# Kernel tuning notes

Hardware: AMD Instinct MI355X
Metric: run time of the kernel (lower is better)

## Reference

```python
import math
import jax, jax.numpy as jnp
import numpy as np

B, N, D = 8, 2048, 256
NUM_ROLES = 3
ROLE_HUB, ROLE_MONITOR = 1, 2  # assumed ROLE_TO_ID mapping
NEG = -10000.0


def _lin_init(k, fan_in, shape):
    b = 1.0 / math.sqrt(fan_in)
    return jax.random.uniform(k, shape, jnp.float32, -b, b)


def setup_inputs() -> dict:
    key = jax.random.key(0)
    ks = jax.random.split(key, 20)
    inp = {
        'x': jax.random.normal(ks[0], (B, N, D), jnp.float32),
        'node_roles': jax.random.randint(ks[1], (B, N), 0, NUM_ROLES),
        'node_mask': jax.random.bernoulli(ks[2], 0.9, (B, N)),
        'ln_gamma': jnp.ones((D,), jnp.float32),
        'ln_beta': jnp.zeros((D,), jnp.float32),
        'role_emb': jax.random.normal(ks[3], (NUM_ROLES, D), jnp.float32),
    }
    names = ['q', 'k', 's', 'p', 'o']
    for i, nm in enumerate(names):
        inp['W' + nm] = _lin_init(ks[4 + 2 * i], D, (D, D))
        inp['b' + nm] = _lin_init(ks[5 + 2 * i], D, (D,))
    inp['Wg'] = _lin_init(ks[14], 2 * D, (2 * D, D))
    inp['bg'] = _lin_init(ks[15], 2 * D, (D,))
    return inp


def _layernorm(x, g, b):
    mu = jnp.mean(x, -1, keepdims=True)
    var = jnp.mean(jnp.square(x - mu), -1, keepdims=True)
    return (x - mu) * jax.lax.rsqrt(var + 1e-5) * g + b


def reference(x, node_roles, node_mask, ln_gamma, ln_beta, role_emb,
              Wq, bq, Wk, bk, Ws, bs, Wp, bp, Wo, bo, Wg, bg):
    normed = _layernorm(x, ln_gamma, ln_beta)
    role_bias = role_emb[node_roles]                      # [B,N,D]
    h = normed + role_bias
    query = h @ Wq + bq
    key_t = h @ Wk + bk
    sender = h @ Ws + bs
    payload = normed @ Wp + bp

    read_logits = jnp.einsum('bid,bjd->bij', query, key_t) / math.sqrt(D)
    fs = role_bias + sender
    forward_logits = jnp.einsum('bid,bjd->bij', fs, fs)
    logits = read_logits + 0.5 * forward_logits           # variant='selective'

    source_mask = node_mask                               # variant != 'memory_hubs'
    pair_mask = node_mask[:, :, None] & source_mask[:, None, :]
    eye = jnp.eye(N, dtype=bool)[None]
    pair_mask = pair_mask | (eye & node_mask[:, :, None] & node_mask[:, None, :])

    logits = jnp.where(pair_mask, logits, NEG)
    weights = jax.nn.softmax(logits, axis=-1)
    weights = jnp.where(pair_mask, weights, 0.0)

    message = jnp.einsum('bij,bjd->bid', weights, payload)
    gate = jax.nn.sigmoid(jnp.concatenate([x, message], axis=-1) @ Wg + bg)
    update = (gate * message) @ Wo + bo
    out = x + update                                      # dropout p=0

    entropy = -(weights * jnp.log(weights + 1e-8)).sum(-1).mean()
    # masked-mean replicates torch's weights[..., col_mask].mean() without dynamic shapes
    mon_cols = (node_roles == ROLE_MONITOR).any(0)        # [N]
    hub_cols = (node_roles == ROLE_HUB).any(0)
    def col_mean(cols):
        cnt = cols.sum() * B * N
        tot = (weights * cols[None, None, :].astype(weights.dtype)).sum()
        return jnp.where(cnt > 0, tot / jnp.maximum(cnt, 1), 0.0)
    return (out, entropy, col_mean(mon_cols), col_mean(hub_cols))
```

## Files before the change

kernel.cpp:

```cpp
#include <hip/hip_runtime.h>
#include <math.h>

#define BB 8
#define NN 2048
#define DD 256
#define MTOK 16384

typedef __bf16 bf16x8 __attribute__((ext_vector_type(8)));
typedef __bf16 bf16x4 __attribute__((ext_vector_type(4)));
typedef float f32x4 __attribute__((ext_vector_type(4)));

#define MFMA16(a, b, c) __builtin_amdgcn_mfma_f32_16x16x32_bf16(a, b, c, 0, 0, 0)

#define BARX()                              \
  do {                                      \
    asm volatile("" ::: "memory");          \
    __builtin_amdgcn_s_barrier();           \
    asm volatile("" ::: "memory");          \
  } while (0)
#define WAITVM(N)                                              \
  do {                                                         \
    asm volatile("s_waitcnt vmcnt(" #N ")" ::: "memory");      \
    __builtin_amdgcn_sched_barrier(0);                         \
  } while (0)

#define OFF_X16    0ull
#define OFF_N16    2097152ull
#define OFF_H16    4194304ull
#define OFF_GROW   8388608ull
#define OFF_GCOL   12582912ull
#define OFF_PTE    16777216ull
#define OFF_WT     19005440ull
#define OFF_STAT   19234816ull
#define OFF_ENT    23625728ull
#define OFF_MONR   23642112ull
#define OFF_HUBR   23658496ull
#define OFF_MONF   23674880ull
#define OFF_HUBF   23676928ull
#define OFF_MASK   23678976ull
#define OFF_PART   23683072ull
#define OFF_MSGN0  OFF_N16
#define OFF_MSGN1  OFF_H16
#define OFF_MSG16  OFF_PTE
#define OFF_GM16   OFF_GROW

__device__ __forceinline__ void gl_lds16(const void* g, void* l) {
  __builtin_amdgcn_global_load_lds(
      (const __attribute__((address_space(1))) unsigned int*)g,
      (__attribute__((address_space(3))) unsigned int*)l, 16, 0, 0);
}

__global__ __launch_bounds__(256) void setup_kernel(
    const float* __restrict__ x, const int* __restrict__ roles,
    const void* __restrict__ mraw,
    const float* __restrict__ gamma, const float* __restrict__ beta,
    const float* __restrict__ role_emb,
    const float* __restrict__ Wq, const float* __restrict__ Wk,
    const float* __restrict__ Ws, const float* __restrict__ Wp,
    const float* __restrict__ Wg, const float* __restrict__ Wo,
    __bf16* __restrict__ X16, __bf16* __restrict__ N16,
    __bf16* __restrict__ H16, __bf16* __restrict__ WT,
    unsigned char* __restrict__ mask8,
    float* __restrict__ monf, float* __restrict__ hubf,
    __bf16* __restrict__ PTE) {
  __shared__ float T[64][65];
  int bid = blockIdx.x;
  int tid = threadIdx.x;
  if (bid < 4096) {
    int t = bid * 4 + (tid >> 6);
    int lane = tid & 63;
    size_t off = (size_t)t * DD + lane * 4;
    float4 xv = *(const float4*)(x + off);
    float s = xv.x + xv.y + xv.z + xv.w;
    float ss = xv.x * xv.x + xv.y * xv.y + xv.z * xv.z + xv.w * xv.w;
#pragma unroll
    for (int m = 1; m < 64; m <<= 1) {
      s += __shfl_xor(s, m, 64);
      ss += __shfl_xor(ss, m, 64);
    }
    float mu = s * (1.0f / 256.0f);
    float var = ss * (1.0f / 256.0f) - mu * mu;
    float inv = rsqrtf(var + 1e-5f);
    float4 g = *(const float4*)(gamma + lane * 4);
    float4 be = *(const float4*)(beta + lane * 4);
    float nv[4];
    nv[0] = (xv.x - mu) * inv * g.x + be.x;
    nv[1] = (xv.y - mu) * inv * g.y + be.y;
    nv[2] = (xv.z - mu) * inv * g.z + be.z;
    nv[3] = (xv.w - mu) * inv * g.w + be.w;
    int role = roles[t];
    float4 rb = *(const float4*)(role_emb + (size_t)role * DD + lane * 4);
    float rbv[4] = {rb.x, rb.y, rb.z, rb.w};
    bf16x4 xo, no, ho;
    float xf[4] = {xv.x, xv.y, xv.z, xv.w};
#pragma unroll
    for (int q = 0; q < 4; ++q) {
      xo[q] = (__bf16)xf[q];
      no[q] = (__bf16)nv[q];
      ho[q] = (__bf16)(nv[q] + rbv[q]);
    }
    *(bf16x4*)&X16[off] = xo;
    *(bf16x4*)&N16[off] = no;
    *(bf16x4*)&H16[off] = ho;
  } else if (bid < 4288) {
    int wblk = bid - 4096;
    int z = wblk >> 5, rem = wblk & 31;
    int bx = rem & 3, by = rem >> 2;
    const float* src;
    int K;
    size_t doff;
    switch (z) {
      case 0: src = Wq; K = 256; doff = 0; break;
      case 1: src = Wk; K = 256; doff = 65536; break;
      case 2: src = Ws; K = 256; doff = 131072; break;
      case 3: src = Wp; K = 256; doff = 196608; break;
      case 4: src = Wg; K = 512; doff = 262144; break;
      default: src = Wo; K = 256; doff = 393216; break;
    }
    int k0 = by * 64;
    if (k0 >= K) return;
    int n0 = bx * 64;
#pragma unroll
    for (int p = 0; p < 16; ++p) {
      int idx = p * 256 + tid;
      int r = idx >> 6, c = idx & 63;
      T[r][c] = src[(size_t)(k0 + r) * 256 + n0 + c];
    }
    __syncthreads();
#pragma unroll
    for (int p = 0; p < 16; ++p) {
      int idx = p * 256 + tid;
      int n = idx >> 6, k = idx & 63;
      WT[doff + (size_t)(n0 + n) * K + k0 + k] = (__bf16)T[k][n];
    }
  } else if (bid < 4352) {
    int* csh = (int*)&T[0][0];
    if (tid == 0) { csh[0] = 0; csh[1] = 0; }
    __syncthreads();
    const unsigned char* raw = (const unsigned char*)mraw;
    int c0 = 0, c1 = 0;
    for (int i = tid; i < 4096; i += 256) {
      int nz = (raw[i] != 0) ? 1 : 0;
      if ((i & 3) == 0) c0 += nz; else c1 += nz;
    }
    atomicAdd(&csh[0], c0);
    atomicAdd(&csh[1], c1);
    __syncthreads();
    int k = (csh[0] == 0) ? 2 : ((csh[1] == 0) ? 0 : 1);
    int t = (bid - 4288) * 256 + tid;
    if (t < MTOK) {
      int v;
      if (k == 1)      v = (raw[t] != 0);
      else if (k == 0) v = (((const int*)mraw)[t] != 0);
      else             v = (((const float*)mraw)[t] != 0.0f);
      mask8[t] = (unsigned char)v;
    }
    if (t < NN) {
      int mon = 0, hub = 0;
#pragma unroll
      for (int b = 0; b < BB; ++b) {
        int r = roles[b * NN + t];
        mon |= (r == 2) ? 1 : 0;
        hub |= (r == 1) ? 1 : 0;
      }
      monf[t] = (float)mon;
      hubf[t] = (float)hub;
    }
  } else {
    int idx = (bid - 4352) * 256 + tid;
    int b = idx >> 11, col = idx & 2047;
    int mon = 0, hub = 0;
#pragma unroll
    for (int bb = 0; bb < BB; ++bb) {
      int r = roles[bb * NN + col];
      mon |= (r == 2) ? 1 : 0;
      hub |= (r == 1) ? 1 : 0;
    }
    size_t rbase = ((size_t)(b * 272 + 256)) * 2048 + col;
    PTE[rbase] = (__bf16)(float)mon;
    PTE[rbase + 2048] = (__bf16)(float)hub;
    PTE[rbase + 2 * 2048] = (__bf16)1.0f;
#pragma unroll
    for (int r = 3; r < 16; ++r) PTE[rbase + (size_t)r * 2048] = (__bf16)0.0f;
  }
}

__global__ __launch_bounds__(256, 4) void proj4_kernel(
    const __bf16* __restrict__ H16, const __bf16* __restrict__ N16,
    const __bf16* __restrict__ WT,
    const float* __restrict__ bq, const float* __restrict__ bk,
    const float* __restrict__ bs, const float* __restrict__ bp,
    const int* __restrict__ roles, const float* __restrict__ remb,
    __bf16* __restrict__ Grow, __bf16* __restrict__ Gcol,
    __bf16* __restrict__ PTE) {
  __shared__ __align__(16) unsigned char As[128 * 128];
  __shared__ __align__(16) unsigned char Bs[128 * 128];
  int z = blockIdx.z;
  const __bf16* A = (z == 3) ? N16 : H16;
  const __bf16* W = WT + (size_t)z * 65536;
  const float* bias = (z == 0) ? bq : (z == 1) ? bk : (z == 2) ? bs : bp;

  int tid = threadIdx.x;
  int w = tid >> 6, lane = tid & 63, ln15 = lane & 15, lq = lane >> 4;
  int wr = w >> 1, wc = w & 1;
  int row0 = blockIdx.y * 128, col0 = blockIdx.x * 128;
  f32x4 acc[4][4];
#pragma unroll
  for (int i = 0; i < 4; ++i)
#pragma unroll
    for (int j = 0; j < 4; ++j) acc[i][j] = (f32x4){0.f, 0.f, 0.f, 0.f};

  int lr = lane >> 3;
  int sb = ((lane & 7) * 16) ^ ((lr & 7) << 4);

  for (int kt = 0; kt < 4; ++kt) {
    __syncthreads();
#pragma unroll
    for (int i2 = 0; i2 < 4; ++i2) {
      int idx = w * 4 + i2;
      int grow = row0 + idx * 8 + lr;
      gl_lds16((const unsigned char*)A + (size_t)grow * 512 + kt * 128 + sb,
               As + idx * 1024);
    }
#pragma unroll
    for (int i2 = 0; i2 < 4; ++i2) {
      int idx = w * 4 + i2;
      int gcol = col0 + idx * 8 + lr;
      gl_lds16((const unsigned char*)W + (size_t)gcol * 512 + kt * 128 + sb,
               Bs + idx * 1024);
    }
    __syncthreads();
#pragma unroll
    for (int ks = 0; ks < 2; ++ks) {
      bf16x8 af[4], bfr[4];
#pragma unroll
      for (int i = 0; i < 4; ++i) {
        int rl = wr * 64 + i * 16 + ln15;
        int byteoff = (lq * 16 + ks * 64) ^ ((rl & 7) << 4);
        af[i] = *(const bf16x8*)(As + rl * 128 + byteoff);
      }
#pragma unroll
      for (int j = 0; j < 4; ++j) {
        int cl = wc * 64 + j * 16 + ln15;
        int byteoff = (lq * 16 + ks * 64) ^ ((cl & 7) << 4);
        bfr[j] = *(const bf16x8*)(Bs + cl * 128 + byteoff);
      }
#pragma unroll
      for (int i = 0; i < 4; ++i)
#pragma unroll
        for (int j = 0; j < 4; ++j) acc[i][j] = MFMA16(af[i], bfr[j], acc[i][j]);
    }
  }
  float bj[4];
#pragma unroll
  for (int j = 0; j < 4; ++j) bj[j] = bias[col0 + wc * 64 + j * 16 + ln15];
#pragma unroll
  for (int i = 0; i < 4; ++i) {
#pragma unroll
    for (int j = 0; j < 4; ++j) {
      int gcol = col0 + wc * 64 + j * 16 + ln15;
      int growb = row0 + wr * 64 + i * 16 + lq * 4;
      float o[4];
#pragma unroll
      for (int ri = 0; ri < 4; ++ri) o[ri] = acc[i][j][ri] + bj[j];
      if (z == 0) {
#pragma unroll
        for (int ri = 0; ri < 4; ++ri)
          Grow[(size_t)(growb + ri) * 512 + gcol] = (__bf16)(o[ri] * 0.0625f);
      } else if (z == 1) {
#pragma unroll
        for (int ri = 0; ri < 4; ++ri)
          Gcol[(size_t)(growb + ri) * 512 + gcol] = (__bf16)o[ri];
      } else if (z == 2) {
#pragma unroll
        for (int ri = 0; ri < 4; ++ri) {
          float oo = o[ri] + remb[(size_t)roles[growb + ri] * 256 + gcol];
          Grow[(size_t)(growb + ri) * 512 + 256 + gcol] =
              (__bf16)(oo * 0.70710678118f);
        }
      } else {
        bf16x4 v;
#pragma unroll
        for (int ri = 0; ri < 4; ++ri) v[ri] = (__bf16)o[ri];
        int b = growb >> 11, tok = growb & 2047;
        *(bf16x4*)&PTE[((size_t)(b * 272 + gcol)) * 2048 + tok] = v;
      }
    }
  }
}

__global__ __launch_bounds__(256, 2) void attn_kernel(
    const __bf16* __restrict__ Grow, const __bf16* __restrict__ Gcol,
    const __bf16* __restrict__ PTE, const unsigned char* __restrict__ mask8,
    __bf16* __restrict__ msgn0, __bf16* __restrict__ msgn1,
    float* __restrict__ statP) {
  __shared__ __align__(16) unsigned char GcLo[16384];
  __shared__ __align__(16) unsigned char GcHi[16384];
  __shared__ __align__(16) unsigned char PtS[2][17408];

  int tid = threadIdx.x;
  int w = tid >> 6, lane = tid & 63, ln15 = lane & 15, lq = lane >> 4;
  int id = blockIdx.x;
  int b = id & 7;
  int half = (id >> 3) & 1;
  int r0 = (id >> 4) * 64;
  size_t base = (size_t)b * NN;
  __bf16* msgn = half ? msgn1 : msgn0;
  float* statB = statP + (size_t)half * MTOK * 6;

  const unsigned char* gbaseK =
      (const unsigned char*)Gcol + (base + half * 1024) * 1024;
  const unsigned char* gbaseF =
      (const unsigned char*)Grow + (base + half * 1024) * 1024;
  const unsigned char* pbase =
      (const unsigned char*)PTE + (size_t)b * 272 * 4096 + half * 2048;

  bf16x8 Af[16];
  {
    const __bf16* gr = Grow + (base + r0 + w * 16 + ln15) * 512 + lq * 8;
#pragma unroll
    for (int kk = 0; kk < 16; ++kk) Af[kk] = *(const bf16x8*)(gr + kk * 32);
  }

  float m = -1e30f, T = 0.f;
  f32x4 macc[17];
#pragma unroll
  for (int nt = 0; nt < 17; ++nt) macc[nt] = (f32x4){0.f, 0.f, 0.f, 0.f};

  int pswz = (lq ^ ((ln15 >> 1) & 3)) << 4;
  int n0 = ((ln15 >> 2) * 8) + (ln15 & 3);
  int n1 = n0 + 4;
  int s0 = (((n0 & 3) | (((n0 >> 3) & 1) << 2))) << 4;
  int s1 = (((n1 & 3) | (((n1 >> 3) & 1) << 2))) << 4;
  int srcsw = ((lane & 3) ^ ((lane >> 3) & 3)) << 4;
  int glrow = lane >> 5;
  int glb = (lane & 31) * 16;

  auto STG = [&](const unsigned char* gb, int ch, unsigned char* dst, int koff) {
#pragma unroll
    for (int i = 0; i < 4; ++i) {
      int rp = w * 8 + 2 * i;
      int r = rp + glrow;
      int sbr = glb ^ ((((r & 3) | (((r >> 3) & 1) << 2))) << 4);
      gl_lds16(gb + (size_t)(ch * 32 + r) * 1024 + koff + sbr, dst + rp * 512);
    }
  };
  auto STPT = [&](int ch, int buf) {
#pragma unroll
    for (int i = 0; i < 4; ++i) {
      int idx = w * 4 + i;
      int drow = idx * 16 + (lane >> 2);
      gl_lds16(pbase + (size_t)drow * 4096 + ch * 64 + srcsw,
               &PtS[buf][idx * 1024]);
    }
    {
      int drow = 256 + (lane >> 2);
      gl_lds16(pbase + (size_t)drow * 4096 + ch * 64 + srcsw,
               &PtS[buf][16 * 1024]);
    }
  };

  STPT(0, 0);
  STG(gbaseK, 0, GcLo, 0);
  STG(gbaseF, 0, GcHi, 512);

  for (int ch = 0; ch < 32; ++ch) {
    int cur = ch & 1;
    WAITVM(4);
    BARX();
    STPT(ch + 1, cur ^ 1);

    f32x4 sa0 = (f32x4){0.f, 0.f, 0.f, 0.f};
    f32x4 sa1 = (f32x4){0.f, 0.f, 0.f, 0.f};
    __builtin_amdgcn_s_setprio(1);
#pragma unroll
    for (int kk = 0; kk < 8; ++kk) {
      bf16x8 bv0 = *(const bf16x8*)&GcLo[n0 * 512 + ((lq * 16 + kk * 64) ^ s0)];
      sa0 = MFMA16(bv0, Af[kk], sa0);
      bf16x8 bv1 = *(const bf16x8*)&GcLo[n1 * 512 + ((lq * 16 + kk * 64) ^ s1)];
      sa1 = MFMA16(bv1, Af[kk], sa1);
    }
    __builtin_amdgcn_s_setprio(0);

    WAITVM(5);
    BARX();
    STG(gbaseK, ch + 1, GcLo, 0);

    __builtin_amdgcn_s_setprio(1);
#pragma unroll
    for (int kk = 8; kk < 16; ++kk) {
      bf16x8 bv0 = *(const bf16x8*)&GcHi[n0 * 512 + ((lq * 16 + (kk - 8) * 64) ^ s0)];
      sa0 = MFMA16(bv0, Af[kk], sa0);
      bf16x8 bv1 = *(const bf16x8*)&GcHi[n1 * 512 + ((lq * 16 + (kk - 8) * 64) ^ s1)];
      sa1 = MFMA16(bv1, Af[kk], sa1);
    }
    __builtin_amdgcn_s_setprio(0);

    float sv[8] = {sa0[0], sa0[1], sa0[2], sa0[3], sa1[0], sa1[1], sa1[2], sa1[3]};
    unsigned long long mk = *(const unsigned long long*)(
        mask8 + base + half * 1024 + (size_t)ch * 32 + lq * 8);

    float mt = -1e30f;
#pragma unroll
    for (int i = 0; i < 8; ++i) {
      float li = ((mk >> (8 * i)) & 0xffull) ? sv[i] : -1e30f;
      mt = fmaxf(mt, li);
    }
    mt = fmaxf(mt, __shfl_xor(mt, 16));
    mt = fmaxf(mt, __shfl_xor(mt, 32));
    float mnew = fmaxf(m, mt);
    if (__any(mnew > m + 8.0f)) {
      float ci = __expf(m - mnew);
      float cir[4];
#pragma unroll
      for (int r = 0; r < 4; ++r)
        cir[r] = __shfl(ci, (lane & 48) + ((lane >> 2) & 12) + r);
#pragma unroll
      for (int nt = 0; nt < 17; ++nt) {
        macc[nt][0] *= cir[0]; macc[nt][1] *= cir[1];
        macc[nt][2] *= cir[2]; macc[nt][3] *= cir[3];
      }
      T *= ci;
      m = mnew;
    }
    float e[8], tl = 0.f;
#pragma unroll
    for (int i = 0; i < 8; ++i) {
      float ei = ((mk >> (8 * i)) & 0xffull) ? __expf(sv[i] - m) : 0.f;
      e[i] = ei;
      tl += ei * sv[i];
    }
    tl += __shfl_xor(tl, 16);
    tl += __shfl_xor(tl, 32);
    T += tl;
    bf16x8 ef;
#pragma unroll
    for (int i = 0; i < 8; ++i) ef[i] = (__bf16)e[i];

    __builtin_amdgcn_s_setprio(1);
#pragma unroll
    for (int nt = 0; nt < 17; ++nt) {
      int drow = nt * 16 + ln15;
      bf16x8 pv = *(const bf16x8*)&PtS[cur][drow * 64 + pswz];
      macc[nt] = MFMA16(ef, pv, macc[nt]);
    }
    __builtin_amdgcn_s_setprio(0);

    BARX();
    STG(gbaseF, ch + 1, GcHi, 512);
  }
  WAITVM(0);

#pragma unroll
  for (int r = 0; r < 4; ++r) {
    int grow = r0 + w * 16 + lq * 4 + r;
    size_t row = base + grow;
    float Z = __shfl(macc[16][r], (lane & 48) + 2);
    float invZ = (Z > 0.f) ? (1.0f / Z) : 0.f;
#pragma unroll
    for (int nt = 0; nt < 16; ++nt)
      msgn[row * 256 + nt * 16 + ln15] = (__bf16)(macc[nt][r] * invZ);
    float Tm = __shfl(macc[16][r], (lane & 48) + 0);
    float Th = __shfl(macc[16][r], (lane & 48) + 1);
    float Tr = __shfl(T, (lane & 48) + ((lane >> 2) & 12) + r);
    float mr = __shfl(m, (lane & 48) + ((lane >> 2) & 12) + r);
    if (ln15 == 0) {
      float* stt = statB + row * 6;
      stt[0] = mr; stt[1] = Tr; stt[2] = Z; stt[3] = Tm; stt[4] = Th;
    }
  }
}

__global__ __launch_bounds__(256) void merge_kernel(
    const __bf16* __restrict__ msgn0, const __bf16* __restrict__ msgn1,
    const float* __restrict__ statP, const unsigned char* __restrict__ mask8,
    __bf16* __restrict__ MSG16, float* __restrict__ entr,
    float* __restrict__ monr, float* __restrict__ hubr) {
  int row = blockIdx.x * 4 + (threadIdx.x >> 6);
  int lane = threadIdx.x & 63;
  const float* s0 = statP + (size_t)row * 6;
  const float* s1 = statP + (size_t)(MTOK + row) * 6;
  float m0 = s0[0], T0 = s0[1], Z0 = s0[2], Tm0 = s0[3], Th0 = s0[4];
  float m1 = s1[0], T1 = s1[1], Z1 = s1[2], Tm1 = s1[3], Th1 = s1[4];
  int valid = mask8[row] != 0;
  float mm = fmaxf(m0, m1);
  float c0 = __expf(m0 - mm), c1 = __expf(m1 - mm);
  float w0 = c0 * Z0, w1 = c1 * Z1;
  float Z = w0 + w1;
  int ok = valid && (Z > 0.f);
  float invZ = ok ? (1.0f / Z) : 0.0f;
  float rw0 = w0 * invZ, rw1 = w1 * invZ;
  bf16x4 p0 = *(const bf16x4*)(msgn0 + (size_t)row * 256 + lane * 4);
  bf16x4 p1 = *(const bf16x4*)(msgn1 + (size_t)row * 256 + lane * 4);
  bf16x4 o;
#pragma unroll
  for (int q = 0; q < 4; ++q)
    o[q] = (__bf16)(rw0 * (float)p0[q] + rw1 * (float)p1[q]);
  *(bf16x4*)&MSG16[(size_t)row * 256 + lane * 4] = o;
  if (lane == 0) {
    float T = c0 * T0 + c1 * T1;
    float Tm = c0 * Tm0 + c1 * Tm1;
    float Th = c0 * Th0 + c1 * Th1;
    entr[row] = ok ? (__logf(Z) + mm - T * invZ) : 0.0f;
    monr[row] = ok ? (Tm * invZ) : 0.0f;
    hubr[row] = ok ? (Th * invZ) : 0.0f;
  }
}

template <int K, int MODE>
__global__ __launch_bounds__(256) void gemmb_kernel(
    const __bf16* __restrict__ A0, const __bf16* __restrict__ A1,
    const __bf16* __restrict__ WT, const float* __restrict__ bias,
    const float* __restrict__ xf, const __bf16* __restrict__ msg16,
    void* __restrict__ dst0) {
  __shared__ __align__(16) unsigned char As[128 * 128];
  __shared__ __align__(16) unsigned char Bs[64 * 128];
  int tid = threadIdx.x;
  int w = tid >> 6, lane = tid & 63, ln15 = lane & 15, lq = lane >> 4;
  int wr = w >> 1, wc = w & 1;
  int row0 = blockIdx.y * 128, col0 = blockIdx.x * 64;
  f32x4 acc[4][2];
#pragma unroll
  for (int i = 0; i < 4; ++i)
#pragma unroll
    for (int j = 0; j < 2; ++j) acc[i][j] = (f32x4){0.f, 0.f, 0.f, 0.f};

  int lr = lane >> 3;
  int sb = ((lane & 7) * 16) ^ ((lr & 7) << 4);

  for (int kt = 0; kt < K / 64; ++kt) {
    const __bf16* Ab = A0;
    int ktl = kt;
    if (K == 512 && kt >= 4) { Ab = A1; ktl = kt - 4; }
    __syncthreads();
#pragma unroll
    for (int i2 = 0; i2 < 4; ++i2) {
      int idx = w * 4 + i2;
      int grow = row0 + idx * 8 + lr;
      gl_lds16((const unsigned char*)Ab + (size_t)grow * 512 + ktl * 128 + sb,
               As + idx * 1024);
    }
#pragma unroll
    for (int i2 = 0; i2 < 2; ++i2) {
      int idx = w * 2 + i2;
      int gcol = col0 + idx * 8 + lr;
      gl_lds16((const unsigned char*)WT + (size_t)gcol * (K * 2) + kt * 128 + sb,
               Bs + idx * 1024);
    }
    __syncthreads();
#pragma unroll
    for (int ks = 0; ks < 2; ++ks) {
      bf16x8 af[4], bfr[2];
#pragma unroll
      for (int i = 0; i < 4; ++i) {
        int rl = wr * 64 + i * 16 + ln15;
        int byteoff = (lq * 16 + ks * 64) ^ ((rl & 7) << 4);
        af[i] = *(const bf16x8*)(As + rl * 128 + byteoff);
      }
#pragma unroll
      for (int j = 0; j < 2; ++j) {
        int cl = wc * 32 + j * 16 + ln15;
        int byteoff = (lq * 16 + ks * 64) ^ ((cl & 7) << 4);
        bfr[j] = *(const bf16x8*)(Bs + cl * 128 + byteoff);
      }
#pragma unroll
      for (int i = 0; i < 4; ++i)
#pragma unroll
        for (int j = 0; j < 2; ++j) acc[i][j] = MFMA16(af[i], bfr[j], acc[i][j]);
    }
  }
  float bj[2];
#pragma unroll
  for (int j = 0; j < 2; ++j) bj[j] = bias[col0 + wc * 32 + j * 16 + ln15];
#pragma unroll
  for (int i = 0; i < 4; ++i) {
#pragma unroll
    for (int ri = 0; ri < 4; ++ri) {
      int grow = row0 + wr * 64 + i * 16 + lq * 4 + ri;
#pragma unroll
      for (int j = 0; j < 2; ++j) {
        int gcol = col0 + wc * 32 + j * 16 + ln15;
        float o = acc[i][j][ri] + bj[j];
        if (MODE == 4) {
          float sg = 1.0f / (1.0f + __expf(-o));
          float mv = (float)msg16[(size_t)grow * 256 + gcol];
          ((__bf16*)dst0)[(size_t)grow * 256 + gcol] = (__bf16)(sg * mv);
        } else {
          ((float*)dst0)[(size_t)grow * 256 + gcol] =
              o + xf[(size_t)grow * 256 + gcol];
        }
      }
    }
  }
}

__device__ __forceinline__ float block_sum(float v, float* sh) {
  __syncthreads();
  sh[threadIdx.x] = v;
  __syncthreads();
  for (int s = 128; s > 0; s >>= 1) {
    if ((int)threadIdx.x < s) sh[threadIdx.x] += sh[threadIdx.x + s];
    __syncthreads();
  }
  return sh[0];
}

__global__ __launch_bounds__(256) void reduce1_kernel(
    const float* __restrict__ entr, const float* __restrict__ monr,
    const float* __restrict__ hubr, float* __restrict__ partial) {
  __shared__ float sh[256];
  int t = blockIdx.x * 256 + threadIdx.x;
  float es = entr[t], ms = monr[t], hs = hubr[t];
  float e = block_sum(es, sh);
  float mo = block_sum(ms, sh);
  float hu = block_sum(hs, sh);
  if (threadIdx.x == 0) {
    partial[blockIdx.x * 4 + 0] = e;
    partial[blockIdx.x * 4 + 1] = mo;
    partial[blockIdx.x * 4 + 2] = hu;
  }
}

__global__ __launch_bounds__(256) void reduce2_kernel(
    const float* __restrict__ partial, const float* __restrict__ monf,
    const float* __restrict__ hubf, float* __restrict__ out3) {
  __shared__ float sh[256];
  float es = 0.f, ms = 0.f, hs = 0.f, cmf = 0.f, chf = 0.f;
  if (threadIdx.x < 64) {
    es = partial[threadIdx.x * 4 + 0];
    ms = partial[threadIdx.x * 4 + 1];
    hs = partial[threadIdx.x * 4 + 2];
  }
  for (int j = threadIdx.x; j < NN; j += 256) { cmf += monf[j]; chf += hubf[j]; }
  float esum = block_sum(es, sh);
  float msum = block_sum(ms, sh);
  float hsum = block_sum(hs, sh);
  float cmsum = block_sum(cmf, sh);
  float chsum = block_sum(chf, sh);
  if (threadIdx.x == 0) {
    out3[0] = esum / 16384.0f;
    out3[1] = (cmsum > 0.f) ? (msum / (cmsum * 16384.0f)) : 0.0f;
    out3[2] = (chsum > 0.f) ? (hsum / (chsum * 16384.0f)) : 0.0f;
  }
}

extern "C" void kernel_launch(void* const* d_in, const int* in_sizes, int n_in,
                              void* d_out, int out_size, void* d_ws, size_t ws_size,
                              hipStream_t stream) {
  const float* x = (const float*)d_in[0];
  const int* roles = (const int*)d_in[1];
  const void* mraw = d_in[2];
  const float* gamma = (const float*)d_in[3];
  const float* beta = (const float*)d_in[4];
  const float* remb = (const float*)d_in[5];
  const float* Wq = (const float*)d_in[6];
  const float* bq = (const float*)d_in[7];
  const float* Wk = (const float*)d_in[8];
  const float* bk = (const float*)d_in[9];
  const float* Ws = (const float*)d_in[10];
  const float* bs = (const float*)d_in[11];
  const float* Wp = (const float*)d_in[12];
  const float* bp = (const float*)d_in[13];
  const float* Wo = (const float*)d_in[14];
  const float* bo = (const float*)d_in[15];
  const float* Wg = (const float*)d_in[16];
  const float* bg = (const float*)d_in[17];

  float* ws = (float*)d_ws;
  __bf16* X16 = (__bf16*)(ws + OFF_X16);
  __bf16* N16 = (__bf16*)(ws + OFF_N16);
  __bf16* H16 = (__bf16*)(ws + OFF_H16);
  __bf16* Grow = (__bf16*)(ws + OFF_GROW);
  __bf16* Gcol = (__bf16*)(ws + OFF_GCOL);
  __bf16* PTE = (__bf16*)(ws + OFF_PTE);
  __bf16* WT = (__bf16*)(ws + OFF_WT);
  float* statP = ws + OFF_STAT;
  __bf16* msgn0 = (__bf16*)(ws + OFF_MSGN0);
  __bf16* msgn1 = (__bf16*)(ws + OFF_MSGN1);
  float* partial = ws + OFF_PART;
  __bf16* MSG16 = (__bf16*)(ws + OFF_MSG16);
  __bf16* GM16 = (__bf16*)(ws + OFF_GM16);
  float* entr = ws + OFF_ENT;
  float* monr = ws + OFF_MONR;
  float* hubr = ws + OFF_HUBR;
  float* monfp = ws + OFF_MONF;
  float* hubfp = ws + OFF_HUBF;
  unsigned char* mask8 = (unsigned char*)(ws + OFF_MASK);
  float* out = (float*)d_out;

  __bf16* WTg = WT + 262144;
  __bf16* WTo = WT + 393216;

  setup_kernel<<<4416, 256, 0, stream>>>(x, roles, mraw, gamma, beta, remb,
                                         Wq, Wk, Ws, Wp, Wg, Wo,
                                         X16, N16, H16, WT, mask8, monfp,
                                         hubfp, PTE);
  proj4_kernel<<<dim3(2, 128, 4), 256, 0, stream>>>(
      H16, N16, WT, bq, bk, bs, bp, roles, remb, Grow, Gcol, PTE);
  attn_kernel<<<512, 256, 0, stream>>>(Grow, Gcol, PTE, mask8, msgn0, msgn1,
                                       statP);
  merge_kernel<<<4096, 256, 0, stream>>>(msgn0, msgn1, statP, mask8, MSG16,
                                         entr, monr, hubr);
  dim3 gg(4, 128);
  gemmb_kernel<512, 4><<<gg, 256, 0, stream>>>(X16, MSG16, WTg, bg, nullptr,
                                               MSG16, GM16);
  gemmb_kernel<256, 5><<<gg, 256, 0, stream>>>(GM16, nullptr, WTo, bo, x,
                                               nullptr, out);
  reduce1_kernel<<<64, 256, 0, stream>>>(entr, monr, hubr, partial);
  reduce2_kernel<<<1, 256, 0, stream>>>(partial, monfp, hubfp, out + 4194304);
}
```

Before: 163.1 us.

## Switch attention kernel to 32x32 MFMA tiles with 128-row blocks and single-barrier staging

Rewrites the attention kernel to use 32x32x16 bf16 MFMA instead of 16x16x32, giving each wave 32 query rows and each block 128 rows, which halves the grid to 256 blocks. Both key and forward-logit tiles and the payload tile are now double-buffered and staged in one call per chunk with a single barrier, instead of split stages. Probability fragments are repacked across lanes with v_permlane32_swap to match the 32x32 B-operand layout. PTE padding grows from 16 to 32 extra rows so the payload fits 9 tiles of 32, and workspace offsets shift accordingly. The intent is fewer MFMA issues and fewer LDS reads per FLOP. The costs are much larger LDS use and register pressure (occupancy 1 block/CU) and only 256 blocks for the device.

```diff
diff --git a/kernel.cpp b/kernel.cpp
--- a/kernel.cpp
+++ b/kernel.cpp
@@ -9,8 +9,10 @@
 typedef __bf16 bf16x8 __attribute__((ext_vector_type(8)));
 typedef __bf16 bf16x4 __attribute__((ext_vector_type(4)));
 typedef float f32x4 __attribute__((ext_vector_type(4)));
+typedef float f32x16 __attribute__((ext_vector_type(16)));
 
 #define MFMA16(a, b, c) __builtin_amdgcn_mfma_f32_16x16x32_bf16(a, b, c, 0, 0, 0)
+#define MFMA32(a, b, c) __builtin_amdgcn_mfma_f32_32x32x16_bf16(a, b, c, 0, 0, 0)
 
 #define BARX()                              \
   do {                                      \
@@ -30,8 +32,8 @@
 #define OFF_GROW   8388608ull
 #define OFF_GCOL   12582912ull
 #define OFF_PTE    16777216ull
-#define OFF_WT     19005440ull
-#define OFF_STAT   19234816ull
+#define OFF_WT     19136512ull
+#define OFF_STAT   19365888ull
 #define OFF_ENT    23625728ull
 #define OFF_MONR   23642112ull
 #define OFF_HUBR   23658496ull
@@ -176,12 +178,12 @@
       mon |= (r == 2) ? 1 : 0;
       hub |= (r == 1) ? 1 : 0;
     }
-    size_t rbase = ((size_t)(b * 272 + 256)) * 2048 + col;
+    size_t rbase = ((size_t)(b * 288 + 256)) * 2048 + col;
     PTE[rbase] = (__bf16)(float)mon;
     PTE[rbase + 2048] = (__bf16)(float)hub;
     PTE[rbase + 2 * 2048] = (__bf16)1.0f;
 #pragma unroll
-    for (int r = 3; r < 16; ++r) PTE[rbase + (size_t)r * 2048] = (__bf16)0.0f;
+    for (int r = 3; r < 32; ++r) PTE[rbase + (size_t)r * 2048] = (__bf16)0.0f;
   }
 }
 
@@ -283,27 +285,29 @@
 #pragma unroll
         for (int ri = 0; ri < 4; ++ri) v[ri] = (__bf16)o[ri];
         int b = growb >> 11, tok = growb & 2047;
-        *(bf16x4*)&PTE[((size_t)(b * 272 + gcol)) * 2048 + tok] = v;
+        *(bf16x4*)&PTE[((size_t)(b * 288 + gcol)) * 2048 + tok] = v;
       }
     }
   }
 }
 
-__global__ __launch_bounds__(256, 2) void attn_kernel(
+__global__ __launch_bounds__(256, 1) void attn_kernel(
     const __bf16* __restrict__ Grow, const __bf16* __restrict__ Gcol,
     const __bf16* __restrict__ PTE, const unsigned char* __restrict__ mask8,
     __bf16* __restrict__ msgn0, __bf16* __restrict__ msgn1,
     float* __restrict__ statP) {
-  __shared__ __align__(16) unsigned char GcLo[16384];
-  __shared__ __align__(16) unsigned char GcHi[16384];
-  __shared__ __align__(16) unsigned char PtS[2][17408];
+  __shared__ __align__(16) unsigned char GcLo[2][16384];
+  __shared__ __align__(16) unsigned char GcHi[2][16384];
+  __shared__ __align__(16) unsigned char PtS[2][36864];
 
   int tid = threadIdx.x;
-  int w = tid >> 6, lane = tid & 63, ln15 = lane & 15, lq = lane >> 4;
+  int w = tid >> 6;
+  int l = tid & 63, l31 = l & 31, hi = l >> 5;
   int id = blockIdx.x;
   int b = id & 7;
   int half = (id >> 3) & 1;
-  int r0 = (id >> 4) * 64;
+  int r0 = (id >> 4) * 128;
+  int q0w = r0 + w * 32;
   size_t base = (size_t)b * NN;
   __bf16* msgn = half ? msgn1 : msgn0;
   float* statB = statP + (size_t)half * MTOK * 6;
@@ -313,158 +317,161 @@
   const unsigned char* gbaseF =
       (const unsigned char*)Grow + (base + half * 1024) * 1024;
   const unsigned char* pbase =
-      (const unsigned char*)PTE + (size_t)b * 272 * 4096 + half * 2048;
-
-  bf16x8 Af[16];
+      (const unsigned char*)PTE + (size_t)b * 288 * 4096 + half * 2048;
+
+  bf16x8 Af[32];
   {
-    const __bf16* gr = Grow + (base + r0 + w * 16 + ln15) * 512 + lq * 8;
-#pragma unroll
-    for (int kk = 0; kk < 16; ++kk) Af[kk] = *(const bf16x8*)(gr + kk * 32);
-  }
+    const __bf16* gr = Grow + (base + q0w + l31) * 512 + hi * 8;
+#pragma unroll
+    for (int ks = 0; ks < 32; ++ks) Af[ks] = *(const bf16x8*)(gr + ks * 16);
+  }
+  WAITVM(0);
 
   float m = -1e30f, T = 0.f;
-  f32x4 macc[17];
-#pragma unroll
-  for (int nt = 0; nt < 17; ++nt) macc[nt] = (f32x4){0.f, 0.f, 0.f, 0.f};
-
-  int pswz = (lq ^ ((ln15 >> 1) & 3)) << 4;
-  int n0 = ((ln15 >> 2) * 8) + (ln15 & 3);
-  int n1 = n0 + 4;
-  int s0 = (((n0 & 3) | (((n0 >> 3) & 1) << 2))) << 4;
-  int s1 = (((n1 & 3) | (((n1 >> 3) & 1) << 2))) << 4;
-  int srcsw = ((lane & 3) ^ ((lane >> 3) & 3)) << 4;
-  int glrow = lane >> 5;
-  int glb = (lane & 31) * 16;
-
-  auto STG = [&](const unsigned char* gb, int ch, unsigned char* dst, int koff) {
+  f32x16 macc[9];
+#pragma unroll
+  for (int t = 0; t < 9; ++t)
+#pragma unroll
+    for (int r = 0; r < 16; ++r) macc[t][r] = 0.f;
+
+  int gsw = (l31 & 7) << 4;
+
+  auto STAGE = [&](int ch, int bufi) {
 #pragma unroll
     for (int i = 0; i < 4; ++i) {
       int rp = w * 8 + 2 * i;
-      int r = rp + glrow;
-      int sbr = glb ^ ((((r & 3) | (((r >> 3) & 1) << 2))) << 4);
-      gl_lds16(gb + (size_t)(ch * 32 + r) * 1024 + koff + sbr, dst + rp * 512);
+      int rl = rp + hi;
+      gl_lds16(gbaseK + (size_t)(ch * 32 + rl) * 1024 +
+                   ((l31 * 16) ^ ((rl & 7) << 4)),
+               &GcLo[bufi][rp * 512]);
+    }
+#pragma unroll
+    for (int i = 0; i < 4; ++i) {
+      int rp = w * 8 + 2 * i;
+      int rl = rp + hi;
+      gl_lds16(gbaseF + (size_t)(ch * 32 + rl) * 1024 + 512 +
+                   ((l31 * 16) ^ ((rl & 7) << 4)),
+               &GcHi[bufi][rp * 512]);
+    }
+#pragma unroll
+    for (int i = 0; i < 9; ++i) {
+      int R = w * 72 + i * 8;
+      int rl = R + (l >> 3);
+      int c = (((l & 7) * 16) ^ ((rl & 7) << 4)) & 63;
+      gl_lds16(pbase + (size_t)rl * 4096 + ch * 64 + c,
+               &PtS[bufi][R * 128]);
     }
   };
-  auto STPT = [&](int ch, int buf) {
-#pragma unroll
-    for (int i = 0; i < 4; ++i) {
-      int idx = w * 4 + i;
-      int drow = idx * 16 + (lane >> 2);
-      gl_lds16(pbase + (size_t)drow * 4096 + ch * 64 + srcsw,
-               &PtS[buf][idx * 1024]);
-    }
-    {
-      int drow = 256 + (lane >> 2);
-      gl_lds16(pbase + (size_t)drow * 4096 + ch * 64 + srcsw,
-               &PtS[buf][16 * 1024]);
-    }
-  };
-
-  STPT(0, 0);
-  STG(gbaseK, 0, GcLo, 0);
-  STG(gbaseF, 0, GcHi, 512);
+
+  STAGE(0, 0);
 
   for (int ch = 0; ch < 32; ++ch) {
-    int cur = ch & 1;
-    WAITVM(4);
+    int buf = ch & 1;
+    STAGE(ch + 1, buf ^ 1);
+    WAITVM(17);
     BARX();
-    STPT(ch + 1, cur ^ 1);
-
-    f32x4 sa0 = (f32x4){0.f, 0.f, 0.f, 0.f};
-    f32x4 sa1 = (f32x4){0.f, 0.f, 0.f, 0.f};
+
+    f32x16 sa;
+#pragma unroll
+    for (int r = 0; r < 16; ++r) sa[r] = 0.f;
     __builtin_amdgcn_s_setprio(1);
 #pragma unroll
-    for (int kk = 0; kk < 8; ++kk) {
-      bf16x8 bv0 = *(const bf16x8*)&GcLo[n0 * 512 + ((lq * 16 + kk * 64) ^ s0)];
-      sa0 = MFMA16(bv0, Af[kk], sa0);
-      bf16x8 bv1 = *(const bf16x8*)&GcLo[n1 * 512 + ((lq * 16 + kk * 64) ^ s1)];
-      sa1 = MFMA16(bv1, Af[kk], sa1);
+    for (int ks = 0; ks < 16; ++ks) {
+      bf16x8 a = *(const bf16x8*)&GcLo[buf][l31 * 512 +
+                                           ((ks * 32 + hi * 16) ^ gsw)];
+      sa = MFMA32(a, Af[ks], sa);
+    }
+#pragma unroll
+    for (int ks = 16; ks < 32; ++ks) {
+      bf16x8 a = *(const bf16x8*)&GcHi[buf][l31 * 512 +
+                                            (((ks - 16) * 32 + hi * 16) ^ gsw)];
+      sa = MFMA32(a, Af[ks], sa);
     }
     __builtin_amdgcn_s_setprio(0);
 
-    WAITVM(5);
-    BARX();
-    STG(gbaseK, ch + 1, GcLo, 0);
-
-    __builtin_amdgcn_s_setprio(1);
-#pragma unroll
-    for (int kk = 8; kk < 16; ++kk) {
-      bf16x8 bv0 = *(const bf16x8*)&GcHi[n0 * 512 + ((lq * 16 + (kk - 8) * 64) ^ s0)];
-      sa0 = MFMA16(bv0, Af[kk], sa0);
-      bf16x8 bv1 = *(const bf16x8*)&GcHi[n1 * 512 + ((lq * 16 + (kk - 8) * 64) ^ s1)];
-      sa1 = MFMA16(bv1, Af[kk], sa1);
-    }
-    __builtin_amdgcn_s_setprio(0);
-
-    float sv[8] = {sa0[0], sa0[1], sa0[2], sa0[3], sa1[0], sa1[1], sa1[2], sa1[3]};
-    unsigned long long mk = *(const unsigned long long*)(
-        mask8 + base + half * 1024 + (size_t)ch * 32 + lq * 8);
-
+    const unsigned long long* mp = (const unsigned long long*)(
+        mask8 + base + half * 1024 + (size_t)ch * 32);
+    unsigned sel[4];
+#pragma unroll
+    for (int j = 0; j < 4; ++j) sel[j] = (unsigned)(mp[j] >> (hi * 32));
+
+    float sv[16];
+    int vld[16];
+#pragma unroll
+    for (int r = 0; r < 16; ++r) {
+      sv[r] = sa[r];
+      vld[r] = (sel[r >> 2] >> (8 * (r & 3))) & 0xff;
+    }
     float mt = -1e30f;
 #pragma unroll
-    for (int i = 0; i < 8; ++i) {
-      float li = ((mk >> (8 * i)) & 0xffull) ? sv[i] : -1e30f;
-      mt = fmaxf(mt, li);
-    }
-    mt = fmaxf(mt, __shfl_xor(mt, 16));
+    for (int r = 0; r < 16; ++r) mt = fmaxf(mt, vld[r] ? sv[r] : -1e30f);
     mt = fmaxf(mt, __shfl_xor(mt, 32));
     float mnew = fmaxf(m, mt);
     if (__any(mnew > m + 8.0f)) {
       float ci = __expf(m - mnew);
-      float cir[4];
-#pragma unroll
-      for (int r = 0; r < 4; ++r)
-        cir[r] = __shfl(ci, (lane & 48) + ((lane >> 2) & 12) + r);
-#pragma unroll
-      for (int nt = 0; nt < 17; ++nt) {
-        macc[nt][0] *= cir[0]; macc[nt][1] *= cir[1];
-        macc[nt][2] *= cir[2]; macc[nt][3] *= cir[3];
-      }
+      float cir[16];
+#pragma unroll
+      for (int r = 0; r < 16; ++r)
+        cir[r] = __shfl(ci, (r & 3) + 8 * (r >> 2) + 4 * hi);
+#pragma unroll
+      for (int t = 0; t < 9; ++t)
+#pragma unroll
+        for (int r = 0; r < 16; ++r) macc[t][r] *= cir[r];
       T *= ci;
       m = mnew;
     }
-    float e[8], tl = 0.f;
-#pragma unroll
-    for (int i = 0; i < 8; ++i) {
-      float ei = ((mk >> (8 * i)) & 0xffull) ? __expf(sv[i] - m) : 0.f;
-      e[i] = ei;
-      tl += ei * sv[i];
-    }
-    tl += __shfl_xor(tl, 16);
+    float e[16], tl = 0.f;
+#pragma unroll
+    for (int r = 0; r < 16; ++r) {
+      float ee = vld[r] ? __expf(sv[r] - m) : 0.f;
+      e[r] = ee;
+      tl += ee * sv[r];
+    }
     tl += __shfl_xor(tl, 32);
     T += tl;
-    bf16x8 ef;
-#pragma unroll
-    for (int i = 0; i < 8; ++i) ef[i] = (__bf16)e[i];
+
+    unsigned wj[8];
+#pragma unroll
+    for (int j = 0; j < 8; ++j)
+      asm("v_cvt_pk_bf16_f32 %0, %1, %2"
+          : "=v"(wj[j]) : "v"(e[2 * j]), "v"(e[2 * j + 1]));
+    asm volatile("v_permlane32_swap_b32 %0, %1" : "+v"(wj[0]), "+v"(wj[2]));
+    asm volatile("v_permlane32_swap_b32 %0, %1" : "+v"(wj[1]), "+v"(wj[3]));
+    asm volatile("v_permlane32_swap_b32 %0, %1" : "+v"(wj[4]), "+v"(wj[6]));
+    asm volatile("v_permlane32_swap_b32 %0, %1" : "+v"(wj[5]), "+v"(wj[7]));
+    union { unsigned u[4]; bf16x8 v; } ue0, ue1;
+    ue0.u[0] = wj[0]; ue0.u[1] = wj[1]; ue0.u[2] = wj[2]; ue0.u[3] = wj[3];
+    ue1.u[0] = wj[4]; ue1.u[1] = wj[5]; ue1.u[2] = wj[6]; ue1.u[3] = wj[7];
+    bf16x8 ef0 = ue0.v, ef1 = ue1.v;
 
     __builtin_amdgcn_s_setprio(1);
 #pragma unroll
-    for (int nt = 0; nt < 17; ++nt) {
-      int drow = nt * 16 + ln15;
-      bf16x8 pv = *(const bf16x8*)&PtS[cur][drow * 64 + pswz];
-      macc[nt] = MFMA16(ef, pv, macc[nt]);
+    for (int t = 0; t < 9; ++t) {
+      const unsigned char* pb = &PtS[buf][(t * 32 + l31) * 128];
+      bf16x8 b0 = *(const bf16x8*)(pb + ((hi * 16) ^ gsw));
+      macc[t] = MFMA32(ef0, b0, macc[t]);
+      bf16x8 b1 = *(const bf16x8*)(pb + ((32 + hi * 16) ^ gsw));
+      macc[t] = MFMA32(ef1, b1, macc[t]);
     }
     __builtin_amdgcn_s_setprio(0);
-
     BARX();
-    STG(gbaseF, ch + 1, GcHi, 512);
   }
   WAITVM(0);
 
 #pragma unroll
-  for (int r = 0; r < 4; ++r) {
-    int grow = r0 + w * 16 + lq * 4 + r;
-    size_t row = base + grow;
-    float Z = __shfl(macc[16][r], (lane & 48) + 2);
+  for (int r = 0; r < 16; ++r) {
+    int qr = (r & 3) + 8 * (r >> 2) + 4 * hi;
+    size_t row = base + q0w + qr;
+    float Z  = __shfl(macc[8][r], (l & 32) + 2);
+    float Tm = __shfl(macc[8][r], (l & 32) + 0);
+    float Th = __shfl(macc[8][r], (l & 32) + 1);
     float invZ = (Z > 0.f) ? (1.0f / Z) : 0.f;
 #pragma unroll
-    for (int nt = 0; nt < 16; ++nt)
-      msgn[row * 256 + nt * 16 + ln15] = (__bf16)(macc[nt][r] * invZ);
-    float Tm = __shfl(macc[16][r], (lane & 48) + 0);
-    float Th = __shfl(macc[16][r], (lane & 48) + 1);
-    float Tr = __shfl(T, (lane & 48) + ((lane >> 2) & 12) + r);
-    float mr = __shfl(m, (lane & 48) + ((lane >> 2) & 12) + r);
-    if (ln15 == 0) {
+    for (int t = 0; t < 8; ++t)
+      msgn[row * 256 + t * 32 + l31] = (__bf16)(macc[t][r] * invZ);
+    float mr = __shfl(m, qr);
+    float Tr = __shfl(T, qr);
+    if (l31 == 0) {
       float* stt = statB + row * 6;
       stt[0] = mr; stt[1] = Tr; stt[2] = Z; stt[3] = Tm; stt[4] = Th;
     }
@@ -697,7 +704,7 @@
                                          hubfp, PTE);
   proj4_kernel<<<dim3(2, 128, 4), 256, 0, stream>>>(
       H16, N16, WT, bq, bk, bs, bp, roles, remb, Grow, Gcol, PTE);
-  attn_kernel<<<512, 256, 0, stream>>>(Grow, Gcol, PTE, mask8, msgn0, msgn1,
+  attn_kernel<<<256, 256, 0, stream>>>(Grow, Gcol, PTE, mask8, msgn0, msgn1,
                                        statP);
   merge_kernel<<<4096, 256, 0, stream>>>(msgn0, msgn1, statP, mask8, MSG16,
                                          entr, monr, hubr);
```

Result: slower. 238.7 us (+46.4%).

## Double-buffer gate/output GEMM LDS tiles and widen column tile to 128

Applied to the files above, without the earlier changes.

The two small epilogue GEMMs now use 128x128 output tiles instead of 128x64, and the grid shrinks from 4x128 to 2x128 blocks. Shared-memory tiles are double-buffered so the next K-slice loads overlap the current MFMA work, with one barrier per iteration instead of two. MFMA sections are wrapped in s_setprio. The aim is better reuse of the A tile and hidden load latency. The cost is more LDS and registers per block, and only 256 blocks on a large GPU, which may leave CUs idle.

```diff
diff --git a/kernel.cpp b/kernel.cpp
--- a/kernel.cpp
+++ b/kernel.cpp
@@ -508,78 +508,86 @@
 }
 
 template <int K, int MODE>
-__global__ __launch_bounds__(256) void gemmb_kernel(
+__global__ __launch_bounds__(256, 2) void gemmb_kernel(
     const __bf16* __restrict__ A0, const __bf16* __restrict__ A1,
     const __bf16* __restrict__ WT, const float* __restrict__ bias,
     const float* __restrict__ xf, const __bf16* __restrict__ msg16,
     void* __restrict__ dst0) {
-  __shared__ __align__(16) unsigned char As[128 * 128];
-  __shared__ __align__(16) unsigned char Bs[64 * 128];
+  __shared__ __align__(16) unsigned char As[2][128 * 128];
+  __shared__ __align__(16) unsigned char Bs[2][128 * 128];
   int tid = threadIdx.x;
   int w = tid >> 6, lane = tid & 63, ln15 = lane & 15, lq = lane >> 4;
   int wr = w >> 1, wc = w & 1;
-  int row0 = blockIdx.y * 128, col0 = blockIdx.x * 64;
-  f32x4 acc[4][2];
+  int row0 = blockIdx.y * 128, col0 = blockIdx.x * 128;
+  f32x4 acc[4][4];
 #pragma unroll
   for (int i = 0; i < 4; ++i)
 #pragma unroll
-    for (int j = 0; j < 2; ++j) acc[i][j] = (f32x4){0.f, 0.f, 0.f, 0.f};
+    for (int j = 0; j < 4; ++j) acc[i][j] = (f32x4){0.f, 0.f, 0.f, 0.f};
 
   int lr = lane >> 3;
   int sb = ((lane & 7) * 16) ^ ((lr & 7) << 4);
 
-  for (int kt = 0; kt < K / 64; ++kt) {
+  auto STAGE = [&](int kt, int bufi) {
     const __bf16* Ab = A0;
     int ktl = kt;
     if (K == 512 && kt >= 4) { Ab = A1; ktl = kt - 4; }
-    __syncthreads();
 #pragma unroll
     for (int i2 = 0; i2 < 4; ++i2) {
       int idx = w * 4 + i2;
       int grow = row0 + idx * 8 + lr;
       gl_lds16((const unsigned char*)Ab + (size_t)grow * 512 + ktl * 128 + sb,
-               As + idx * 1024);
-    }
-#pragma unroll
-    for (int i2 = 0; i2 < 2; ++i2) {
-      int idx = w * 2 + i2;
+               &As[bufi][idx * 1024]);
+    }
+#pragma unroll
+    for (int i2 = 0; i2 < 4; ++i2) {
+      int idx = w * 4 + i2;
       int gcol = col0 + idx * 8 + lr;
       gl_lds16((const unsigned char*)WT + (size_t)gcol * (K * 2) + kt * 128 + sb,
-               Bs + idx * 1024);
-    }
-    __syncthreads();
+               &Bs[bufi][idx * 1024]);
+    }
+  };
+
+  STAGE(0, 0);
+  for (int kt = 0; kt < K / 64; ++kt) {
+    int buf = kt & 1;
+    WAITVM(0);
+    BARX();
+    if (kt + 1 < K / 64) STAGE(kt + 1, buf ^ 1);
 #pragma unroll
     for (int ks = 0; ks < 2; ++ks) {
-      bf16x8 af[4], bfr[2];
+      bf16x8 af[4], bfr[4];
 #pragma unroll
       for (int i = 0; i < 4; ++i) {
         int rl = wr * 64 + i * 16 + ln15;
         int byteoff = (lq * 16 + ks * 64) ^ ((rl & 7) << 4);
-        af[i] = *(const bf16x8*)(As + rl * 128 + byteoff);
+        af[i] = *(const bf16x8*)&As[buf][rl * 128 + byteoff];
       }
 #pragma unroll
-      for (int j = 0; j < 2; ++j) {
-        int cl = wc * 32 + j * 16 + ln15;
+      for (int j = 0; j < 4; ++j) {
+        int cl = wc * 64 + j * 16 + ln15;
         int byteoff = (lq * 16 + ks * 64) ^ ((cl & 7) << 4);
-        bfr[j] = *(const bf16x8*)(Bs + cl * 128 + byteoff);
+        bfr[j] = *(const bf16x8*)&Bs[buf][cl * 128 + byteoff];
       }
+      __builtin_amdgcn_s_setprio(1);
 #pragma unroll
       for (int i = 0; i < 4; ++i)
 #pragma unroll
-        for (int j = 0; j < 2; ++j) acc[i][j] = MFMA16(af[i], bfr[j], acc[i][j]);
-    }
-  }
-  float bj[2];
-#pragma unroll
-  for (int j = 0; j < 2; ++j) bj[j] = bias[col0 + wc * 32 + j * 16 + ln15];
+        for (int j = 0; j < 4; ++j) acc[i][j] = MFMA16(af[i], bfr[j], acc[i][j]);
+      __builtin_amdgcn_s_setprio(0);
+    }
+  }
+  float bj[4];
+#pragma unroll
+  for (int j = 0; j < 4; ++j) bj[j] = bias[col0 + wc * 64 + j * 16 + ln15];
 #pragma unroll
   for (int i = 0; i < 4; ++i) {
 #pragma unroll
     for (int ri = 0; ri < 4; ++ri) {
       int grow = row0 + wr * 64 + i * 16 + lq * 4 + ri;
 #pragma unroll
-      for (int j = 0; j < 2; ++j) {
-        int gcol = col0 + wc * 32 + j * 16 + ln15;
+      for (int j = 0; j < 4; ++j) {
+        int gcol = col0 + wc * 64 + j * 16 + ln15;
         float o = acc[i][j][ri] + bj[j];
         if (MODE == 4) {
           float sg = 1.0f / (1.0f + __expf(-o));
@@ -701,11 +709,10 @@
                                        statP);
   merge_kernel<<<4096, 256, 0, stream>>>(msgn0, msgn1, statP, mask8, MSG16,
                                          entr, monr, hubr);
-  dim3 gg(4, 128);
-  gemmb_kernel<512, 4><<<gg, 256, 0, stream>>>(X16, MSG16, WTg, bg, nullptr,
-                                               MSG16, GM16);
-  gemmb_kernel<256, 5><<<gg, 256, 0, stream>>>(GM16, nullptr, WTo, bo, x,
-                                               nullptr, out);
+  gemmb_kernel<512, 4><<<dim3(2, 128), 256, 0, stream>>>(
+      X16, MSG16, WTg, bg, nullptr, MSG16, GM16);
+  gemmb_kernel<256, 5><<<dim3(2, 128), 256, 0, stream>>>(
+      GM16, nullptr, WTo, bo, x, nullptr, out);
   reduce1_kernel<<<64, 256, 0, stream>>>(entr, monr, hubr, partial);
   reduce2_kernel<<<1, 256, 0, stream>>>(partial, monfp, hubfp, out + 4194304);
 }
```

New measurement: 164.2 us. No clear change (+0.7%).
